# Optimization experiments

Measured on AMD Instinct MI355X. Metric: run time of the kernel, lower is better.

Reference implementation:

```python
import jax, jax.numpy as jnp
import numpy as np


def setup_inputs() -> dict:
    key = jax.random.key(0)
    k1, k2 = jax.random.split(key)
    b, c, h, w = 16, 512, 64, 64
    rgb_feat = jax.random.normal(k1, (b, c, h, w), dtype=jnp.float32)
    depth_feat = jax.random.normal(k2, (b, c, h, w), dtype=jnp.float32)
    return {"rgb_feat": rgb_feat, "depth_feat": depth_feat}


def reference(rgb_feat, depth_feat):
    b, c, h, w = rgb_feat.shape
    rgb_r = rgb_feat.reshape(b, c, h * w)      # (b, c, hw)
    depth_r = depth_feat.reshape(b, c, h * w)  # (b, c, hw)
    # interaction: (b, c, c) = depth_r @ rgb_r^T
    interaction = jnp.einsum('bcs,bds->bcd', depth_r, rgb_r)
    interaction = jax.nn.sigmoid(interaction)
    # depth_weighted: (b, c, hw) = interaction @ depth_r
    depth_weighted = jnp.einsum('bcd,bds->bcs', interaction, depth_r)
    fused = rgb_feat + depth_weighted.reshape(b, c, h, w)
    return fused
```

## Files before the change

kernel.cpp:

```cpp
#include <hip/hip_runtime.h>

#define B_ 16
#define C_ 512
#define S_ 4096

typedef __attribute__((ext_vector_type(4))) float float4v;
typedef __attribute__((ext_vector_type(8))) short short8;
typedef __attribute__((ext_vector_type(4))) short short4v;

typedef __attribute__((address_space(1))) unsigned int as1_uint;
typedef __attribute__((address_space(3))) unsigned int as3_uint;

#define ASYNC16(gsrc, ldst) \
  __builtin_amdgcn_global_load_lds((as1_uint*)(gsrc), (as3_uint*)(ldst), 16, 0, 0)

__device__ __forceinline__ unsigned short f2bf(float f) {
  unsigned u = __builtin_bit_cast(unsigned, f);
  u = u + 0x7FFFu + ((u >> 16) & 1u);
  return (unsigned short)(u >> 16);
}

__global__ __launch_bounds__(256) void k_transpose(
    const float* __restrict__ depth, unsigned short* __restrict__ depthT) {
  __shared__ float tile[64][129];
  int b = blockIdx.z;
  int s0 = blockIdx.x * 64, d0 = blockIdx.y * 128;
  int t = threadIdx.x;
  const float* src = depth + (b * C_ + d0) * S_ + s0;
#pragma unroll
  for (int it = 0; it < 8; ++it) {
    int slot = it * 256 + t;
    int d = slot >> 4, l16 = slot & 15;
    float4v v = *(const float4v*)(src + d * S_ + l16 * 4);
    tile[l16 * 4 + 0][d] = v.x;
    tile[l16 * 4 + 1][d] = v.y;
    tile[l16 * 4 + 2][d] = v.z;
    tile[l16 * 4 + 3][d] = v.w;
  }
  __syncthreads();
  unsigned short* dst = depthT + (b * S_ + s0) * C_ + d0;
#pragma unroll
  for (int it = 0; it < 8; ++it) {
    int slot = it * 256 + t;
    int s = slot >> 5, l32 = slot & 31;
    float x0 = tile[s][l32 * 4 + 0];
    float x1 = tile[s][l32 * 4 + 1];
    float x2 = tile[s][l32 * 4 + 2];
    float x3 = tile[s][l32 * 4 + 3];
    short4v o = {(short)f2bf(x0), (short)f2bf(x1), (short)f2bf(x2), (short)f2bf(x3)};
    *(short4v*)(dst + s * C_ + l32 * 4) = o;
  }
}

__global__ __launch_bounds__(256) void k_gemm1(
    const float* __restrict__ depth, const float* __restrict__ rgb,
    float* __restrict__ partial) {
  const int BK = 32, LDA = 40;
  __shared__ __align__(16) short As[128 * LDA];
  __shared__ __align__(16) short Bs[128 * LDA];
  int bz = blockIdx.z;
  int b = bz >> 2, ks = bz & 3;
  int c0 = blockIdx.x * 128, d0 = blockIdx.y * 128;
  int t = threadIdx.x;
  const float* Abase = depth + (size_t)(b * C_ + c0) * S_ + ks * 1024;
  const float* Bbase = rgb + (size_t)(b * C_ + d0) * S_ + ks * 1024;
  int w = t >> 6, l = t & 63, half = l >> 4, r = l & 15;
  int wm = (w >> 1) * 64, wn = (w & 1) * 64;

  float4v acc[4][4] = {};
  float4v pa[4], pb[4];

#pragma unroll
  for (int q = 0; q < 4; ++q) {
    int idx = q * 256 + t, row = idx >> 3, ch = idx & 7;
    pa[q] = *(const float4v*)(Abase + row * S_ + ch * 4);
    pb[q] = *(const float4v*)(Bbase + row * S_ + ch * 4);
  }

  const int NKT = 1024 / BK;
  for (int kt = 0; kt < NKT; ++kt) {
#pragma unroll
    for (int q = 0; q < 4; ++q) {
      int idx = q * 256 + t, row = idx >> 3, ch = idx & 7;
      short4v sa = {(short)f2bf(pa[q].x), (short)f2bf(pa[q].y),
                    (short)f2bf(pa[q].z), (short)f2bf(pa[q].w)};
      short4v sb = {(short)f2bf(pb[q].x), (short)f2bf(pb[q].y),
                    (short)f2bf(pb[q].z), (short)f2bf(pb[q].w)};
      *(short4v*)&As[row * LDA + ch * 4] = sa;
      *(short4v*)&Bs[row * LDA + ch * 4] = sb;
    }
    __syncthreads();
    if (kt + 1 < NKT) {
      int k0 = (kt + 1) * BK;
#pragma unroll
      for (int q = 0; q < 4; ++q) {
        int idx = q * 256 + t, row = idx >> 3, ch = idx & 7;
        pa[q] = *(const float4v*)(Abase + row * S_ + k0 + ch * 4);
        pb[q] = *(const float4v*)(Bbase + row * S_ + k0 + ch * 4);
      }
    }
    short8 af[4], bfr[4];
#pragma unroll
    for (int i = 0; i < 4; ++i)
      af[i] = *(const short8*)&As[(wm + 16 * i + r) * LDA + half * 8];
#pragma unroll
    for (int j = 0; j < 4; ++j)
      bfr[j] = *(const short8*)&Bs[(wn + 16 * j + r) * LDA + half * 8];
#pragma unroll
    for (int i = 0; i < 4; ++i)
#pragma unroll
      for (int j = 0; j < 4; ++j)
        acc[i][j] =
            __builtin_amdgcn_mfma_f32_16x16x32_bf16(af[i], bfr[j], acc[i][j], 0, 0, 0);
    __syncthreads();
  }

  float* P = partial + ((size_t)(ks * B_ + b) * C_) * C_;
#pragma unroll
  for (int i = 0; i < 4; ++i)
#pragma unroll
    for (int j = 0; j < 4; ++j)
#pragma unroll
      for (int reg = 0; reg < 4; ++reg) {
        int c = c0 + wm + 16 * i + half * 4 + reg;
        int d = d0 + wn + 16 * j + r;
        P[(size_t)c * C_ + d] = acc[i][j][reg];
      }
}

__global__ __launch_bounds__(256) void k_reduce(const float* __restrict__ p,
                                                unsigned short* __restrict__ I) {
  const size_t n = (size_t)B_ * C_ * C_;
  size_t idx = ((size_t)blockIdx.x * 256 + threadIdx.x) * 4;
  float4v s = *(const float4v*)(p + idx);
  s += *(const float4v*)(p + n + idx);
  s += *(const float4v*)(p + 2 * n + idx);
  s += *(const float4v*)(p + 3 * n + idx);
  float g0 = 1.0f / (1.0f + __expf(-s.x));
  float g1 = 1.0f / (1.0f + __expf(-s.y));
  float g2 = 1.0f / (1.0f + __expf(-s.z));
  float g3 = 1.0f / (1.0f + __expf(-s.w));
  short4v o = {(short)f2bf(g0), (short)f2bf(g1), (short)f2bf(g2), (short)f2bf(g3)};
  *(short4v*)(I + idx) = o;
}

__global__ __launch_bounds__(256) void k_gemm2(
    const unsigned short* __restrict__ I, const unsigned short* __restrict__ depthT,
    const float* __restrict__ rgb, float* __restrict__ out) {
  const int BK = 32;
  __shared__ __align__(16) short As[128 * BK];
  __shared__ __align__(16) short Bs[128 * BK];
  int b = blockIdx.z;
  int c0 = blockIdx.x * 128, s0 = blockIdx.y * 128;
  int t = threadIdx.x;
  const unsigned short* Ab = I + (size_t)(b * C_ + c0) * C_;
  const unsigned short* Bb = depthT + (size_t)(b * S_ + s0) * C_;
  int w = t >> 6, l = t & 63, half = l >> 4, r = l & 15;
  int wm = (w >> 1) * 64, wn = (w & 1) * 64;
  float4v acc[4][4] = {};

  for (int k0 = 0; k0 < C_; k0 += BK) {
    __syncthreads();
#pragma unroll
    for (int q = 0; q < 2; ++q) {
      int idx = q * 256 + t;
      ASYNC16(Ab + (idx >> 2) * C_ + k0 + (idx & 3) * 8, &As[idx * 8]);
    }
#pragma unroll
    for (int q = 0; q < 2; ++q) {
      int idx = q * 256 + t;
      ASYNC16(Bb + (idx >> 2) * C_ + k0 + (idx & 3) * 8, &Bs[idx * 8]);
    }
    __syncthreads();

    short8 af[4], bfr[4];
#pragma unroll
    for (int i = 0; i < 4; ++i)
      af[i] = *(const short8*)&As[(wm + 16 * i + r) * BK + half * 8];
#pragma unroll
    for (int j = 0; j < 4; ++j)
      bfr[j] = *(const short8*)&Bs[(wn + 16 * j + r) * BK + half * 8];
#pragma unroll
    for (int i = 0; i < 4; ++i)
#pragma unroll
      for (int j = 0; j < 4; ++j)
        acc[i][j] =
            __builtin_amdgcn_mfma_f32_16x16x32_bf16(af[i], bfr[j], acc[i][j], 0, 0, 0);
  }

#pragma unroll
  for (int i = 0; i < 4; ++i)
#pragma unroll
    for (int j = 0; j < 4; ++j)
#pragma unroll
      for (int reg = 0; reg < 4; ++reg) {
        int c = c0 + wm + 16 * i + half * 4 + reg;
        int s = s0 + wn + 16 * j + r;
        size_t o = (size_t)(b * C_ + c) * S_ + s;
        out[o] = rgb[o] + acc[i][j][reg];
      }
}

extern "C" void kernel_launch(void* const* d_in, const int* in_sizes, int n_in,
                              void* d_out, int out_size, void* d_ws, size_t ws_size,
                              hipStream_t stream) {
  const float* rgb = (const float*)d_in[0];
  const float* depth = (const float*)d_in[1];
  float* out = (float*)d_out;
  unsigned short* depthT = (unsigned short*)d_ws;
  unsigned short* I = (unsigned short*)((char*)d_ws + (size_t)B_ * S_ * C_ * 2);
  float* partial = out;

  k_transpose<<<dim3(S_ / 64, C_ / 128, B_), 256, 0, stream>>>(depth, depthT);
  k_gemm1<<<dim3(C_ / 128, C_ / 128, B_ * 4), 256, 0, stream>>>(depth, rgb, partial);
  k_reduce<<<dim3((B_ * C_ * C_) / 1024), 256, 0, stream>>>(partial, I);
  k_gemm2<<<dim3(C_ / 128, S_ / 128, B_), 256, 0, stream>>>(I, depthT, rgb, out);
}
```

Baseline: 493.8 us.

## Pre-convert inputs to bf16, drop split-K reduce, double-buffer swizzled async GEMMs

The prep kernel now writes bf16 copies of depth and rgb, keeping the transposed depth as before, into the output buffer used as scratch. gemm1 reads those copies with async global-to-LDS loads and XOR-swizzled shared tiles. It also drops the 4-way split-K and applies the sigmoid in its epilogue, which removes the partial buffer and the reduce kernel. Both GEMMs now double-buffer 64-wide K tiles so the next tile loads while the current one computes. The cost is an extra bf16 write and re-read of both inputs, plus fewer blocks in gemm1 with a long K loop.

```diff
diff --git a/kernel.cpp b/kernel.cpp
--- a/kernel.cpp
+++ b/kernel.cpp
@@ -20,25 +20,38 @@
   return (unsigned short)(u >> 16);
 }
 
-__global__ __launch_bounds__(256) void k_transpose(
-    const float* __restrict__ depth, unsigned short* __restrict__ depthT) {
+__global__ __launch_bounds__(256) void k_prep(
+    const float* __restrict__ depth, const float* __restrict__ rgb,
+    unsigned short* __restrict__ depthN, unsigned short* __restrict__ rgbN,
+    unsigned short* __restrict__ depthT) {
   __shared__ float tile[64][129];
   int b = blockIdx.z;
   int s0 = blockIdx.x * 64, d0 = blockIdx.y * 128;
   int t = threadIdx.x;
-  const float* src = depth + (b * C_ + d0) * S_ + s0;
+  size_t base = ((size_t)(b * C_ + d0)) * S_ + s0;
+  const float* dsrc = depth + base;
+  const float* rsrc = rgb + base;
+  unsigned short* dN = depthN + base;
+  unsigned short* rN = rgbN + base;
 #pragma unroll
   for (int it = 0; it < 8; ++it) {
     int slot = it * 256 + t;
     int d = slot >> 4, l16 = slot & 15;
-    float4v v = *(const float4v*)(src + d * S_ + l16 * 4);
+    float4v v = *(const float4v*)(dsrc + d * S_ + l16 * 4);
     tile[l16 * 4 + 0][d] = v.x;
     tile[l16 * 4 + 1][d] = v.y;
     tile[l16 * 4 + 2][d] = v.z;
     tile[l16 * 4 + 3][d] = v.w;
+    short4v o = {(short)f2bf(v.x), (short)f2bf(v.y), (short)f2bf(v.z),
+                 (short)f2bf(v.w)};
+    *(short4v*)(dN + d * S_ + l16 * 4) = o;
+    float4v u = *(const float4v*)(rsrc + d * S_ + l16 * 4);
+    short4v o2 = {(short)f2bf(u.x), (short)f2bf(u.y), (short)f2bf(u.z),
+                  (short)f2bf(u.w)};
+    *(short4v*)(rN + d * S_ + l16 * 4) = o2;
   }
   __syncthreads();
-  unsigned short* dst = depthT + (b * S_ + s0) * C_ + d0;
+  unsigned short* dT = depthT + ((size_t)(b * S_ + s0)) * C_ + d0;
 #pragma unroll
   for (int it = 0; it < 8; ++it) {
     int slot = it * 256 + t;
@@ -47,145 +60,143 @@
     float x1 = tile[s][l32 * 4 + 1];
     float x2 = tile[s][l32 * 4 + 2];
     float x3 = tile[s][l32 * 4 + 3];
-    short4v o = {(short)f2bf(x0), (short)f2bf(x1), (short)f2bf(x2), (short)f2bf(x3)};
-    *(short4v*)(dst + s * C_ + l32 * 4) = o;
+    short4v o = {(short)f2bf(x0), (short)f2bf(x1), (short)f2bf(x2),
+                 (short)f2bf(x3)};
+    *(short4v*)(dT + s * C_ + l32 * 4) = o;
   }
 }
 
 __global__ __launch_bounds__(256) void k_gemm1(
-    const float* __restrict__ depth, const float* __restrict__ rgb,
-    float* __restrict__ partial) {
-  const int BK = 32, LDA = 40;
-  __shared__ __align__(16) short As[128 * LDA];
-  __shared__ __align__(16) short Bs[128 * LDA];
-  int bz = blockIdx.z;
-  int b = bz >> 2, ks = bz & 3;
-  int c0 = blockIdx.x * 128, d0 = blockIdx.y * 128;
+    const unsigned short* __restrict__ depthN,
+    const unsigned short* __restrict__ rgbN, unsigned short* __restrict__ I) {
+  __shared__ __align__(16) short As[2][64 * 64];
+  __shared__ __align__(16) short Bs[2][128 * 64];
+  int b = blockIdx.z;
+  int c0 = blockIdx.x * 64, d0 = blockIdx.y * 128;
   int t = threadIdx.x;
-  const float* Abase = depth + (size_t)(b * C_ + c0) * S_ + ks * 1024;
-  const float* Bbase = rgb + (size_t)(b * C_ + d0) * S_ + ks * 1024;
+  const unsigned short* An = depthN + ((size_t)(b * C_ + c0)) * S_;
+  const unsigned short* Bn = rgbN + ((size_t)(b * C_ + d0)) * S_;
   int w = t >> 6, l = t & 63, half = l >> 4, r = l & 15;
-  int wm = (w >> 1) * 64, wn = (w & 1) * 64;
-
-  float4v acc[4][4] = {};
-  float4v pa[4], pb[4];
-
-#pragma unroll
-  for (int q = 0; q < 4; ++q) {
-    int idx = q * 256 + t, row = idx >> 3, ch = idx & 7;
-    pa[q] = *(const float4v*)(Abase + row * S_ + ch * 4);
-    pb[q] = *(const float4v*)(Bbase + row * S_ + ch * 4);
-  }
-
-  const int NKT = 1024 / BK;
+  int wm = (w >> 1) * 32, wn = (w & 1) * 64;
+  float4v acc[2][4] = {};
+
+  auto stage = [&](int bi, int k0) {
+#pragma unroll
+    for (int q = 0; q < 2; ++q) {
+      int idx = q * 256 + t, row = idx >> 3, ch = (idx & 7) ^ (row & 7);
+      ASYNC16(An + (size_t)row * S_ + k0 + ch * 8, &As[bi][idx * 8]);
+    }
+#pragma unroll
+    for (int q = 0; q < 4; ++q) {
+      int idx = q * 256 + t, row = idx >> 3, ch = (idx & 7) ^ (row & 7);
+      ASYNC16(Bn + (size_t)row * S_ + k0 + ch * 8, &Bs[bi][idx * 8]);
+    }
+  };
+
+  stage(0, 0);
+  __syncthreads();
+  const int NKT = S_ / 64;
   for (int kt = 0; kt < NKT; ++kt) {
-#pragma unroll
-    for (int q = 0; q < 4; ++q) {
-      int idx = q * 256 + t, row = idx >> 3, ch = idx & 7;
-      short4v sa = {(short)f2bf(pa[q].x), (short)f2bf(pa[q].y),
-                    (short)f2bf(pa[q].z), (short)f2bf(pa[q].w)};
-      short4v sb = {(short)f2bf(pb[q].x), (short)f2bf(pb[q].y),
-                    (short)f2bf(pb[q].z), (short)f2bf(pb[q].w)};
-      *(short4v*)&As[row * LDA + ch * 4] = sa;
-      *(short4v*)&Bs[row * LDA + ch * 4] = sb;
-    }
-    __syncthreads();
-    if (kt + 1 < NKT) {
-      int k0 = (kt + 1) * BK;
-#pragma unroll
-      for (int q = 0; q < 4; ++q) {
-        int idx = q * 256 + t, row = idx >> 3, ch = idx & 7;
-        pa[q] = *(const float4v*)(Abase + row * S_ + k0 + ch * 4);
-        pb[q] = *(const float4v*)(Bbase + row * S_ + k0 + ch * 4);
-      }
-    }
-    short8 af[4], bfr[4];
-#pragma unroll
-    for (int i = 0; i < 4; ++i)
-      af[i] = *(const short8*)&As[(wm + 16 * i + r) * LDA + half * 8];
-#pragma unroll
-    for (int j = 0; j < 4; ++j)
-      bfr[j] = *(const short8*)&Bs[(wn + 16 * j + r) * LDA + half * 8];
-#pragma unroll
-    for (int i = 0; i < 4; ++i)
-#pragma unroll
-      for (int j = 0; j < 4; ++j)
-        acc[i][j] =
-            __builtin_amdgcn_mfma_f32_16x16x32_bf16(af[i], bfr[j], acc[i][j], 0, 0, 0);
-    __syncthreads();
-  }
-
-  float* P = partial + ((size_t)(ks * B_ + b) * C_) * C_;
-#pragma unroll
-  for (int i = 0; i < 4; ++i)
+    int cur = kt & 1;
+    if (kt + 1 < NKT) stage(cur ^ 1, (kt + 1) * 64);
+    short8 af[2][2], bfr[4][2];
+#pragma unroll
+    for (int i = 0; i < 2; ++i) {
+      int row = wm + 16 * i + r;
+#pragma unroll
+      for (int kk = 0; kk < 2; ++kk)
+        af[i][kk] =
+            *(const short8*)&As[cur][row * 64 +
+                                     (((kk * 4 + half) ^ (row & 7)) * 8)];
+    }
+#pragma unroll
+    for (int j = 0; j < 4; ++j) {
+      int row = wn + 16 * j + r;
+#pragma unroll
+      for (int kk = 0; kk < 2; ++kk)
+        bfr[j][kk] =
+            *(const short8*)&Bs[cur][row * 64 +
+                                     (((kk * 4 + half) ^ (row & 7)) * 8)];
+    }
+#pragma unroll
+    for (int kk = 0; kk < 2; ++kk)
+#pragma unroll
+      for (int i = 0; i < 2; ++i)
+#pragma unroll
+        for (int j = 0; j < 4; ++j)
+          acc[i][j] = __builtin_amdgcn_mfma_f32_16x16x32_bf16(
+              af[i][kk], bfr[j][kk], acc[i][j], 0, 0, 0);
+    if (kt + 1 < NKT) __syncthreads();
+  }
+
+#pragma unroll
+  for (int i = 0; i < 2; ++i)
 #pragma unroll
     for (int j = 0; j < 4; ++j)
 #pragma unroll
       for (int reg = 0; reg < 4; ++reg) {
         int c = c0 + wm + 16 * i + half * 4 + reg;
         int d = d0 + wn + 16 * j + r;
-        P[(size_t)c * C_ + d] = acc[i][j][reg];
+        float g = 1.0f / (1.0f + __expf(-acc[i][j][reg]));
+        I[((size_t)(b * C_ + c)) * C_ + d] = f2bf(g);
       }
 }
 
-__global__ __launch_bounds__(256) void k_reduce(const float* __restrict__ p,
-                                                unsigned short* __restrict__ I) {
-  const size_t n = (size_t)B_ * C_ * C_;
-  size_t idx = ((size_t)blockIdx.x * 256 + threadIdx.x) * 4;
-  float4v s = *(const float4v*)(p + idx);
-  s += *(const float4v*)(p + n + idx);
-  s += *(const float4v*)(p + 2 * n + idx);
-  s += *(const float4v*)(p + 3 * n + idx);
-  float g0 = 1.0f / (1.0f + __expf(-s.x));
-  float g1 = 1.0f / (1.0f + __expf(-s.y));
-  float g2 = 1.0f / (1.0f + __expf(-s.z));
-  float g3 = 1.0f / (1.0f + __expf(-s.w));
-  short4v o = {(short)f2bf(g0), (short)f2bf(g1), (short)f2bf(g2), (short)f2bf(g3)};
-  *(short4v*)(I + idx) = o;
-}
-
 __global__ __launch_bounds__(256) void k_gemm2(
-    const unsigned short* __restrict__ I, const unsigned short* __restrict__ depthT,
-    const float* __restrict__ rgb, float* __restrict__ out) {
-  const int BK = 32;
-  __shared__ __align__(16) short As[128 * BK];
-  __shared__ __align__(16) short Bs[128 * BK];
+    const unsigned short* __restrict__ I,
+    const unsigned short* __restrict__ depthT, const float* __restrict__ rgb,
+    float* __restrict__ out) {
+  __shared__ __align__(16) short As[2][128 * 64];
+  __shared__ __align__(16) short Bs[2][128 * 64];
   int b = blockIdx.z;
   int c0 = blockIdx.x * 128, s0 = blockIdx.y * 128;
   int t = threadIdx.x;
-  const unsigned short* Ab = I + (size_t)(b * C_ + c0) * C_;
-  const unsigned short* Bb = depthT + (size_t)(b * S_ + s0) * C_;
+  const unsigned short* Ab = I + ((size_t)(b * C_ + c0)) * C_;
+  const unsigned short* Bb = depthT + ((size_t)(b * S_ + s0)) * C_;
   int w = t >> 6, l = t & 63, half = l >> 4, r = l & 15;
   int wm = (w >> 1) * 64, wn = (w & 1) * 64;
   float4v acc[4][4] = {};
 
-  for (int k0 = 0; k0 < C_; k0 += BK) {
-    __syncthreads();
-#pragma unroll
-    for (int q = 0; q < 2; ++q) {
-      int idx = q * 256 + t;
-      ASYNC16(Ab + (idx >> 2) * C_ + k0 + (idx & 3) * 8, &As[idx * 8]);
-    }
-#pragma unroll
-    for (int q = 0; q < 2; ++q) {
-      int idx = q * 256 + t;
-      ASYNC16(Bb + (idx >> 2) * C_ + k0 + (idx & 3) * 8, &Bs[idx * 8]);
-    }
-    __syncthreads();
-
-    short8 af[4], bfr[4];
-#pragma unroll
-    for (int i = 0; i < 4; ++i)
-      af[i] = *(const short8*)&As[(wm + 16 * i + r) * BK + half * 8];
-#pragma unroll
-    for (int j = 0; j < 4; ++j)
-      bfr[j] = *(const short8*)&Bs[(wn + 16 * j + r) * BK + half * 8];
-#pragma unroll
-    for (int i = 0; i < 4; ++i)
-#pragma unroll
-      for (int j = 0; j < 4; ++j)
-        acc[i][j] =
-            __builtin_amdgcn_mfma_f32_16x16x32_bf16(af[i], bfr[j], acc[i][j], 0, 0, 0);
+  auto stage = [&](int bi, int k0) {
+#pragma unroll
+    for (int q = 0; q < 4; ++q) {
+      int idx = q * 256 + t, row = idx >> 3, ch = (idx & 7) ^ (row & 7);
+      ASYNC16(Ab + (size_t)row * C_ + k0 + ch * 8, &As[bi][idx * 8]);
+      ASYNC16(Bb + (size_t)row * C_ + k0 + ch * 8, &Bs[bi][idx * 8]);
+    }
+  };
+
+  stage(0, 0);
+  __syncthreads();
+  const int NKT = C_ / 64;
+  for (int kt = 0; kt < NKT; ++kt) {
+    int cur = kt & 1;
+    if (kt + 1 < NKT) stage(cur ^ 1, (kt + 1) * 64);
+    short8 af[4][2], bfr[4][2];
+#pragma unroll
+    for (int i = 0; i < 4; ++i) {
+      int rowa = wm + 16 * i + r;
+#pragma unroll
+      for (int kk = 0; kk < 2; ++kk)
+        af[i][kk] =
+            *(const short8*)&As[cur][rowa * 64 +
+                                     (((kk * 4 + half) ^ (rowa & 7)) * 8)];
+      int rowb = wn + 16 * i + r;
+#pragma unroll
+      for (int kk = 0; kk < 2; ++kk)
+        bfr[i][kk] =
+            *(const short8*)&Bs[cur][rowb * 64 +
+                                     (((kk * 4 + half) ^ (rowb & 7)) * 8)];
+    }
+#pragma unroll
+    for (int kk = 0; kk < 2; ++kk)
+#pragma unroll
+      for (int i = 0; i < 4; ++i)
+#pragma unroll
+        for (int j = 0; j < 4; ++j)
+          acc[i][j] = __builtin_amdgcn_mfma_f32_16x16x32_bf16(
+              af[i][kk], bfr[j][kk], acc[i][j], 0, 0, 0);
+    if (kt + 1 < NKT) __syncthreads();
   }
 
 #pragma unroll
@@ -196,23 +207,26 @@
       for (int reg = 0; reg < 4; ++reg) {
         int c = c0 + wm + 16 * i + half * 4 + reg;
         int s = s0 + wn + 16 * j + r;
-        size_t o = (size_t)(b * C_ + c) * S_ + s;
+        size_t o = ((size_t)(b * C_ + c)) * S_ + s;
         out[o] = rgb[o] + acc[i][j][reg];
       }
 }
 
 extern "C" void kernel_launch(void* const* d_in, const int* in_sizes, int n_in,
-                              void* d_out, int out_size, void* d_ws, size_t ws_size,
-                              hipStream_t stream) {
+                              void* d_out, int out_size, void* d_ws,
+                              size_t ws_size, hipStream_t stream) {
   const float* rgb = (const float*)d_in[0];
   const float* depth = (const float*)d_in[1];
   float* out = (float*)d_out;
   unsigned short* depthT = (unsigned short*)d_ws;
-  unsigned short* I = (unsigned short*)((char*)d_ws + (size_t)B_ * S_ * C_ * 2);
-  float* partial = out;
-
-  k_transpose<<<dim3(S_ / 64, C_ / 128, B_), 256, 0, stream>>>(depth, depthT);
-  k_gemm1<<<dim3(C_ / 128, C_ / 128, B_ * 4), 256, 0, stream>>>(depth, rgb, partial);
-  k_reduce<<<dim3((B_ * C_ * C_) / 1024), 256, 0, stream>>>(partial, I);
-  k_gemm2<<<dim3(C_ / 128, S_ / 128, B_), 256, 0, stream>>>(I, depthT, rgb, out);
-}
+  unsigned short* I =
+      (unsigned short*)((char*)d_ws + (size_t)B_ * S_ * C_ * 2);
+  unsigned short* depthN = (unsigned short*)d_out;
+  unsigned short* rgbN = depthN + (size_t)B_ * C_ * S_;
+
+  k_prep<<<dim3(S_ / 64, C_ / 128, B_), 256, 0, stream>>>(depth, rgb, depthN,
+                                                          rgbN, depthT);
+  k_gemm1<<<dim3(C_ / 64, C_ / 128, B_), 256, 0, stream>>>(depthN, rgbN, I);
+  k_gemm2<<<dim3(C_ / 128, S_ / 128, B_), 256, 0, stream>>>(I, depthT, rgb,
+                                                            out);
+}
```

New measurement: 502.8 us. About the same (+1.8%).
